# Performance work log

Hardware: AMD Instinct MI355X
Metric: run time of the kernel (lower is better)

The kernel has to match this reference:

```python
import jax, jax.numpy as jnp
import numpy as np

K = 31  # AvgPool2d kernel size
P = 15  # padding


def _box_avg(x):
    """31x31 stride-1 avg pool, count_include_pad=True (PyTorch default):
    separable ones-conv with zero padding, divided by K*K."""
    B, C, H, W = x.shape
    kh = jnp.ones((C, 1, K, 1), x.dtype)
    kw = jnp.ones((C, 1, 1, K), x.dtype)
    dn = ('NCHW', 'OIHW', 'NCHW')
    y = jax.lax.conv_general_dilated(x, kh, (1, 1), [(P, P), (0, 0)],
                                     dimension_numbers=dn, feature_group_count=C)
    y = jax.lax.conv_general_dilated(y, kw, (1, 1), [(0, 0), (P, P)],
                                     dimension_numbers=dn, feature_group_count=C)
    return y / (K * K)


def setup_inputs() -> dict:
    key = jax.random.key(0)
    k1, k2 = jax.random.split(key)
    pred = jax.random.normal(k1, (64, 1, 512, 512), dtype=jnp.float32)
    mask = jax.random.uniform(k2, (64, 1, 512, 512), dtype=jnp.float32)
    return {"pred": pred, "mask": mask}


def reference(pred, mask):
    weit = 1.0 + 5.0 * jnp.abs(_box_avg(mask) - mask)
    p = jax.nn.sigmoid(pred)
    inter = jnp.sum(p * mask * weit, axis=(2, 3))          # [B, C]
    union = jnp.sum((p + mask) * weit, axis=(2, 3))        # [B, C]
    wdiss = 1.0 - (2.0 * inter + 0.5) / (union + 0.5)
    return jnp.mean(wdiss)
```

## Files before the change

### kernel.cpp

```cpp
#include <hip/hip_runtime.h>
#include <math.h>

#define NB 64
#define HH 512
#define WW 512
#define KK 31
#define PP 15
#define TS 32
#define NSTRIP (HH / TS)
#define HR (TS + KK - 1)
#define NPAIR (HR / 2)

typedef _Float16 f16;
typedef f16 f16x8 __attribute__((ext_vector_type(8)));
typedef f16 f16x4 __attribute__((ext_vector_type(4)));
typedef f16 f16x2 __attribute__((ext_vector_type(2)));

__device__ __forceinline__ f16x2 shfl_up2(f16x2 v, int delta) {
    int x = __shfl_up(__builtin_bit_cast(int, v), delta);
    return __builtin_bit_cast(f16x2, x);
}
__device__ __forceinline__ f16x2 shfl_dn2(f16x2 v, int delta) {
    int x = __shfl_down(__builtin_bit_cast(int, v), delta);
    return __builtin_bit_cast(f16x2, x);
}
__device__ __forceinline__ f16x2 sel2(bool c, f16x2 v) {
    f16x2 z = {(f16)0, (f16)0};
    return c ? v : z;
}


__global__ __launch_bounds__(512, 4) void dice_fused_kernel(
        const float* __restrict__ pred,
        const float* __restrict__ mask,
        float* __restrict__ part) {
    const int strip = blockIdx.x;
    const int b     = blockIdx.y;
    const int t     = threadIdx.x;
    const int wave  = t >> 6;
    const int lane  = t & 63;

    __shared__ f16 Hs[HR][WW];
    __shared__ float red[16];

    const float* mb = mask + (size_t)b * HH * WW;
    const float* pb = pred + (size_t)b * HH * WW;
    const int y0 = strip * TS;

    const int xbase = lane * 8;
    const bool lm1 = (lane >= 1);
    const bool lm2 = (lane >= 2);
    const bool lp1 = (lane <= 62);
    const bool lp2 = (lane <= 61);

    float va[4][8], vb[4][8];
    #pragma unroll
    for (int k = 0; k < 4; ++k) {
        const int p = k * 8 + wave;
        const int gya = y0 + 2 * p - PP;
        const int gyb = gya + 1;
        const bool pa = (p < NPAIR) && (gya >= 0) && (gya < HH);
        const bool qb = (p < NPAIR) && (gyb >= 0) && (gyb < HH);
        if (pa) {
            const float* row = mb + (size_t)gya * WW + xbase;
            const float4 u = *(const float4*)(row);
            const float4 v = *(const float4*)(row + 4);
            va[k][0] = u.x; va[k][1] = u.y; va[k][2] = u.z; va[k][3] = u.w;
            va[k][4] = v.x; va[k][5] = v.y; va[k][6] = v.z; va[k][7] = v.w;
        } else {
            #pragma unroll
            for (int j = 0; j < 8; ++j) va[k][j] = 0.0f;
        }
        if (qb) {
            const float* row = mb + (size_t)gyb * WW + xbase;
            const float4 u = *(const float4*)(row);
            const float4 v = *(const float4*)(row + 4);
            vb[k][0] = u.x; vb[k][1] = u.y; vb[k][2] = u.z; vb[k][3] = u.w;
            vb[k][4] = v.x; vb[k][5] = v.y; vb[k][6] = v.z; vb[k][7] = v.w;
        } else {
            #pragma unroll
            for (int j = 0; j < 8; ++j) vb[k][j] = 0.0f;
        }
    }

    #pragma unroll
    for (int k = 0; k < 4; ++k) {
        const int p = k * 8 + wave;
        if (p >= NPAIR) continue;
        const int ra = 2 * p;
        const int rb = ra + 1;

        float sa[8], sb[8];
        sa[0] = va[k][0]; sb[0] = vb[k][0];
        #pragma unroll
        for (int j = 1; j < 8; ++j) { sa[j] = sa[j-1] + va[k][j]; sb[j] = sb[j-1] + vb[k][j]; }

        f16x2 ps[8];
        #pragma unroll
        for (int j = 0; j < 8; ++j) { ps[j][0] = (f16)sa[j]; ps[j][1] = (f16)sb[j]; }
        const f16x2 pT = ps[7];

        f16x2 A[7];
        #pragma unroll
        for (int j = 0; j < 7; ++j) A[j] = shfl_up2(pT - ps[j], 2);
        const f16x2 Bprev = shfl_up2(pT, 1);
        const f16x2 Cfull = shfl_dn2(pT, 1);
        f16x2 Cp[7];
        #pragma unroll
        for (int j = 0; j < 7; ++j) Cp[j] = shfl_dn2(ps[j], 2);

        f16x2 base = pT;
        base += sel2(lm1, Bprev);
        base += sel2(lp1, Cfull);

        f16x8 ha, hb;
        #pragma unroll
        for (int j = 0; j < 8; ++j) {
            f16x2 acc = base;
            if (j < 7) acc += sel2(lm2, A[j]);
            if (j > 0) acc += sel2(lp2, Cp[j-1]);
            ha[j] = acc[0];
            hb[j] = acc[1];
        }
        *(f16x8*)&Hs[ra][xbase] = ha;
        *(f16x8*)&Hs[rb][xbase] = hb;
    }
    __syncthreads();

    const int q  = t & 127;
    const int g  = t >> 7;
    const int c  = q * 4;
    const int r0 = g * 8;

    float4 M[8], Pq[8];
    #pragma unroll
    for (int i = 0; i < 8; ++i) {
        const int y = y0 + r0 + i;
        M[i]  = *(const float4*)(mb + (size_t)y * WW + c);
        Pq[i] = *(const float4*)(pb + (size_t)y * WW + c);
    }

    float4 B = make_float4(0.f, 0.f, 0.f, 0.f);
    #pragma unroll
    for (int j = 0; j < KK - 1; ++j) {
        const f16x4 h = *(const f16x4*)&Hs[r0 + j][c];
        B.x += (float)h[0]; B.y += (float)h[1]; B.z += (float)h[2]; B.w += (float)h[3];
    }

    float4 I4 = make_float4(0.f, 0.f, 0.f, 0.f);
    float4 U4 = make_float4(0.f, 0.f, 0.f, 0.f);
    const float inv2 = 1.0f / (float)(KK * KK);

    #pragma unroll
    for (int i = 0; i < 8; ++i) {
        const f16x4 he = *(const f16x4*)&Hs[r0 + i + (KK - 1)][c];
        const f16x4 hl = *(const f16x4*)&Hs[r0 + i][c];
        const float4 m4 = M[i];
        const float4 p4 = Pq[i];

        B.x += (float)he[0]; B.y += (float)he[1]; B.z += (float)he[2]; B.w += (float)he[3];

        const float w0 = 1.0f + 5.0f * fabsf(B.x * inv2 - m4.x);
        const float w1 = 1.0f + 5.0f * fabsf(B.y * inv2 - m4.y);
        const float w2 = 1.0f + 5.0f * fabsf(B.z * inv2 - m4.z);
        const float w3 = 1.0f + 5.0f * fabsf(B.w * inv2 - m4.w);
        const float sg0 = 1.0f / (1.0f + __expf(-p4.x));
        const float sg1 = 1.0f / (1.0f + __expf(-p4.y));
        const float sg2 = 1.0f / (1.0f + __expf(-p4.z));
        const float sg3 = 1.0f / (1.0f + __expf(-p4.w));

        I4.x += sg0 * m4.x * w0;  U4.x += (sg0 + m4.x) * w0;
        I4.y += sg1 * m4.y * w1;  U4.y += (sg1 + m4.y) * w1;
        I4.z += sg2 * m4.z * w2;  U4.z += (sg2 + m4.z) * w2;
        I4.w += sg3 * m4.w * w3;  U4.w += (sg3 + m4.w) * w3;

        B.x -= (float)hl[0]; B.y -= (float)hl[1]; B.z -= (float)hl[2]; B.w -= (float)hl[3];
    }

    float inter = I4.x + I4.y + I4.z + I4.w;
    float uni   = U4.x + U4.y + U4.z + U4.w;
    #pragma unroll
    for (int off = 32; off > 0; off >>= 1) {
        inter += __shfl_down(inter, off);
        uni   += __shfl_down(uni, off);
    }
    if (lane == 0) { red[wave] = inter; red[8 + wave] = uni; }
    __syncthreads();
    if (t == 0) {
        float ti = 0.f, tu = 0.f;
        #pragma unroll
        for (int w2 = 0; w2 < 8; ++w2) { ti += red[w2]; tu += red[8 + w2]; }
        const int bid = b * NSTRIP + strip;
        part[bid] = ti;
        part[NB * NSTRIP + bid] = tu;
    }
}

__global__ void dice_final_kernel(const float* __restrict__ part,
                                  float* __restrict__ out) {
    const int t = threadIdx.x;
    float inter = 0.0f, uni = 0.0f;
    #pragma unroll
    for (int s = 0; s < NSTRIP; ++s) {
        inter += part[t * NSTRIP + s];
        uni   += part[NB * NSTRIP + t * NSTRIP + s];
    }
    float wd = 1.0f - (2.0f * inter + 0.5f) / (uni + 0.5f);
    #pragma unroll
    for (int off = 32; off > 0; off >>= 1) wd += __shfl_down(wd, off);
    if (t == 0) out[0] = wd * (1.0f / (float)NB);
}

extern "C" void kernel_launch(void* const* d_in, const int* in_sizes, int n_in,
                              void* d_out, int out_size, void* d_ws, size_t ws_size,
                              hipStream_t stream) {
    const float* pred = (const float*)d_in[0];
    const float* mask = (const float*)d_in[1];
    float* out  = (float*)d_out;
    float* part = (float*)d_ws;

    dim3 grid(NSTRIP, NB);
    dice_fused_kernel<<<grid, 512, 0, stream>>>(pred, mask, part);
    dice_final_kernel<<<1, 64, 0, stream>>>(part, out);
}
```

Before: 149.8 us.

## Prefetch pred/mask tiles before horizontal pass and batch LDS column sums

Issues the global loads of the mask and pred tiles before the horizontal box-sum phase, using empty asm to pin them in registers so their latency overlaps the shuffle work and the barrier. The vertical-sum prologue now loads all needed LDS rows up front and accumulates in packed fp16 with two partial accumulators. It also uses packed round-toward-zero conversion, fma forms and a hardware reciprocal for the sigmoid. This raises register pressure under the 512x4 launch bounds, which risks spills, and fp16 accumulation of 15-row sums slightly reduces precision.

```diff
diff --git a/kernel.cpp b/kernel.cpp
--- a/kernel.cpp
+++ b/kernel.cpp
@@ -28,6 +28,9 @@
     f16x2 z = {(f16)0, (f16)0};
     return c ? v : z;
 }
+__device__ __forceinline__ void keep4(float4& v) {
+    asm volatile("" : "+v"(v.x), "+v"(v.y), "+v"(v.z), "+v"(v.w));
+}
 
 
 __global__ __launch_bounds__(512, 4) void dice_fused_kernel(
@@ -47,12 +50,12 @@
     const float* pb = pred + (size_t)b * HH * WW;
     const int y0 = strip * TS;
 
+    const int q  = t & 127;
+    const int g  = t >> 7;
+    const int c  = q * 4;
+    const int r0 = g * 8;
+
     const int xbase = lane * 8;
-    const bool lm1 = (lane >= 1);
-    const bool lm2 = (lane >= 2);
-    const bool lp1 = (lane <= 62);
-    const bool lp2 = (lane <= 61);
-
     float va[4][8], vb[4][8];
     #pragma unroll
     for (int k = 0; k < 4; ++k) {
@@ -83,6 +86,21 @@
         }
     }
 
+    float4 M[8], Pq[8];
+    #pragma unroll
+    for (int i = 0; i < 8; ++i) {
+        const int y = y0 + r0 + i;
+        M[i]  = *(const float4*)(mb + (size_t)y * WW + c);
+        Pq[i] = *(const float4*)(pb + (size_t)y * WW + c);
+    }
+    #pragma unroll
+    for (int i = 0; i < 8; ++i) { keep4(M[i]); keep4(Pq[i]); }
+
+    const bool lm1 = (lane >= 1);
+    const bool lm2 = (lane >= 2);
+    const bool lp1 = (lane <= 62);
+    const bool lp2 = (lane <= 61);
+
     #pragma unroll
     for (int k = 0; k < 4; ++k) {
         const int p = k * 8 + wave;
@@ -97,7 +115,8 @@
 
         f16x2 ps[8];
         #pragma unroll
-        for (int j = 0; j < 8; ++j) { ps[j][0] = (f16)sa[j]; ps[j][1] = (f16)sb[j]; }
+        for (int j = 0; j < 8; ++j)
+            ps[j] = __builtin_bit_cast(f16x2, __builtin_amdgcn_cvt_pkrtz(sa[j], sb[j]));
         const f16x2 pT = ps[7];
 
         f16x2 A[7];
@@ -127,25 +146,26 @@
     }
     __syncthreads();
 
-    const int q  = t & 127;
-    const int g  = t >> 7;
-    const int c  = q * 4;
-    const int r0 = g * 8;
-
-    float4 M[8], Pq[8];
-    #pragma unroll
-    for (int i = 0; i < 8; ++i) {
-        const int y = y0 + r0 + i;
-        M[i]  = *(const float4*)(mb + (size_t)y * WW + c);
-        Pq[i] = *(const float4*)(pb + (size_t)y * WW + c);
-    }
-
-    float4 B = make_float4(0.f, 0.f, 0.f, 0.f);
-    #pragma unroll
-    for (int j = 0; j < KK - 1; ++j) {
-        const f16x4 h = *(const f16x4*)&Hs[r0 + j][c];
-        B.x += (float)h[0]; B.y += (float)h[1]; B.z += (float)h[2]; B.w += (float)h[3];
-    }
+    f16x4 hl8[8], he8[8];
+    f16x4 accA = {(f16)0, (f16)0, (f16)0, (f16)0};
+    f16x4 accB = {(f16)0, (f16)0, (f16)0, (f16)0};
+    #pragma unroll
+    for (int j = 0; j < 8; ++j) {
+        hl8[j] = *(const f16x4*)&Hs[r0 + j][c];
+        accA += hl8[j];
+    }
+    #pragma unroll
+    for (int j = 8; j < 15; ++j) accA += *(const f16x4*)&Hs[r0 + j][c];
+    #pragma unroll
+    for (int j = 15; j < 30; ++j) accB += *(const f16x4*)&Hs[r0 + j][c];
+    #pragma unroll
+    for (int i = 0; i < 8; ++i) he8[i] = *(const f16x4*)&Hs[r0 + 30 + i][c];
+
+    float4 B;
+    B.x = (float)accA[0] + (float)accB[0];
+    B.y = (float)accA[1] + (float)accB[1];
+    B.z = (float)accA[2] + (float)accB[2];
+    B.w = (float)accA[3] + (float)accB[3];
 
     float4 I4 = make_float4(0.f, 0.f, 0.f, 0.f);
     float4 U4 = make_float4(0.f, 0.f, 0.f, 0.f);
@@ -153,26 +173,26 @@
 
     #pragma unroll
     for (int i = 0; i < 8; ++i) {
-        const f16x4 he = *(const f16x4*)&Hs[r0 + i + (KK - 1)][c];
-        const f16x4 hl = *(const f16x4*)&Hs[r0 + i][c];
+        const f16x4 he = he8[i];
+        const f16x4 hl = hl8[i];
         const float4 m4 = M[i];
         const float4 p4 = Pq[i];
 
         B.x += (float)he[0]; B.y += (float)he[1]; B.z += (float)he[2]; B.w += (float)he[3];
 
-        const float w0 = 1.0f + 5.0f * fabsf(B.x * inv2 - m4.x);
-        const float w1 = 1.0f + 5.0f * fabsf(B.y * inv2 - m4.y);
-        const float w2 = 1.0f + 5.0f * fabsf(B.z * inv2 - m4.z);
-        const float w3 = 1.0f + 5.0f * fabsf(B.w * inv2 - m4.w);
-        const float sg0 = 1.0f / (1.0f + __expf(-p4.x));
-        const float sg1 = 1.0f / (1.0f + __expf(-p4.y));
-        const float sg2 = 1.0f / (1.0f + __expf(-p4.z));
-        const float sg3 = 1.0f / (1.0f + __expf(-p4.w));
-
-        I4.x += sg0 * m4.x * w0;  U4.x += (sg0 + m4.x) * w0;
-        I4.y += sg1 * m4.y * w1;  U4.y += (sg1 + m4.y) * w1;
-        I4.z += sg2 * m4.z * w2;  U4.z += (sg2 + m4.z) * w2;
-        I4.w += sg3 * m4.w * w3;  U4.w += (sg3 + m4.w) * w3;
+        const float w0 = fmaf(5.0f, fabsf(fmaf(B.x, inv2, -m4.x)), 1.0f);
+        const float w1 = fmaf(5.0f, fabsf(fmaf(B.y, inv2, -m4.y)), 1.0f);
+        const float w2 = fmaf(5.0f, fabsf(fmaf(B.z, inv2, -m4.z)), 1.0f);
+        const float w3 = fmaf(5.0f, fabsf(fmaf(B.w, inv2, -m4.w)), 1.0f);
+        const float sg0 = __builtin_amdgcn_rcpf(1.0f + __expf(-p4.x));
+        const float sg1 = __builtin_amdgcn_rcpf(1.0f + __expf(-p4.y));
+        const float sg2 = __builtin_amdgcn_rcpf(1.0f + __expf(-p4.z));
+        const float sg3 = __builtin_amdgcn_rcpf(1.0f + __expf(-p4.w));
+
+        I4.x = fmaf(sg0 * m4.x, w0, I4.x);  U4.x = fmaf(sg0 + m4.x, w0, U4.x);
+        I4.y = fmaf(sg1 * m4.y, w1, I4.y);  U4.y = fmaf(sg1 + m4.y, w1, U4.y);
+        I4.z = fmaf(sg2 * m4.z, w2, I4.z);  U4.z = fmaf(sg2 + m4.z, w2, U4.z);
+        I4.w = fmaf(sg3 * m4.w, w3, I4.w);  U4.w = fmaf(sg3 + m4.w, w3, U4.w);
 
         B.x -= (float)hl[0]; B.y -= (float)hl[1]; B.z -= (float)hl[2]; B.w -= (float)hl[3];
     }
```

Result: slower. 191.9 us (+28.1%).
